# Kernel optimization log

Measured on AMD Instinct MI355X. Metric: run time of the kernel, lower is better.

## Reference

```python
import jax, jax.numpy as jnp
import numpy as np

B, S, D, H = 2, 2048, 1024, 16
DK = D // H


def setup_inputs() -> dict:
    key = jax.random.key(0)
    ks = jax.random.split(key, 9)
    w_scale = 0.02  # small init for linear weights
    return {
        "query": jax.random.normal(ks[0], (B, S, D), jnp.float32),
        "key": jax.random.normal(ks[1], (B, S, D), jnp.float32),
        "value": jax.random.normal(ks[2], (B, S, D), jnp.float32),
        "mask": jax.random.randint(ks[3], (B, 1, S, S), 0, 2).astype(bool),
        "Wq": jax.random.normal(ks[4], (D, D), jnp.float32) * w_scale,
        "bq": jnp.zeros((D,), jnp.float32),
        "Wk": jax.random.normal(ks[5], (D, D), jnp.float32) * w_scale,
        "bk": jnp.zeros((D,), jnp.float32),
        "Wv": jax.random.normal(ks[6], (D, D), jnp.float32) * w_scale,
        "bv": jnp.zeros((D,), jnp.float32),
        "Wo": jax.random.normal(ks[7], (D, D), jnp.float32) * w_scale,
        "bo": jnp.zeros((D,), jnp.float32),
    }


def _split_heads(x):
    # [B,S,D] -> [B,H,S,DK]
    return x.reshape(B, S, H, DK).transpose(0, 2, 1, 3)


def reference(query, key, value, mask, Wq, bq, Wk, bk, Wv, bv, Wo, bo):
    Q = _split_heads(query @ Wq + bq)
    K = _split_heads(key @ Wk + bk)
    V = _split_heads(value @ Wv + bv)
    scores = jnp.einsum("bhqd,bhkd->bhqk", Q, K) / jnp.sqrt(jnp.float32(DK))
    scores = jnp.where(mask, -jnp.inf, scores)  # masked_fill(mask, -inf)
    attn_w = jax.nn.softmax(scores, axis=-1)
    attn_w = jnp.nan_to_num(attn_w, nan=0.0)  # rows fully masked -> 0
    out = jnp.einsum("bhqk,bhkd->bhqd", attn_w, V)
    out = out.transpose(0, 2, 1, 3).reshape(B, S, D)
    return out @ Wo + bo
```

## Files before the change

kernel.cpp:

```cpp
#include <hip/hip_runtime.h>
#include <hip/hip_bf16.h>
#include <cmath>
#include <cstdint>
#include <cstddef>

#define B_  2
#define S_  2048
#define D_  1024
#define H_  16
#define DK_ 64
#define NEG_BIG (-1e30f)
#define QSCALE 0.1803368801111204f

typedef __attribute__((ext_vector_type(8))) short bf16x8;
typedef __attribute__((ext_vector_type(4))) float f32x4;
typedef __attribute__((ext_vector_type(16))) float f32x16;

static __device__ __forceinline__ unsigned short f2bf(float f) {
  __hip_bfloat16 h = __float2bfloat16(f);
  return *reinterpret_cast<unsigned short*>(&h);
}

static __device__ __forceinline__ unsigned cvtpk(float lo, float hi) {
  unsigned d;
  asm("v_cvt_pk_bf16_f32 %0, %1, %2" : "=v"(d) : "v"(lo), "v"(hi));
  return d;
}
static __device__ __forceinline__ float vexp2(float x) {
  float r;
  asm("v_exp_f32 %0, %1" : "=v"(r) : "v"(x));
  return r;
}
#define SWAP32(a, b) asm("v_permlane32_swap_b32 %0, %1" : "+v"(a), "+v"(b))

typedef __attribute__((address_space(3))) unsigned int lds_u32;
typedef __attribute__((address_space(1))) const unsigned int glb_u32;

__global__ void pack_mask_kernel(const int* __restrict__ mask,
                                 unsigned* __restrict__ bits) {
  const int t = blockIdx.x * 256 + threadIdx.x;
  const unsigned long long ball = __ballot(mask[t] != 0);
  const int lane = threadIdx.x & 63;
  if ((lane & 31) == 0)
    bits[t >> 5] = (lane == 0) ? (unsigned)ball : (unsigned)(ball >> 32);
}

__global__ __launch_bounds__(256) void transpose_w_kernel(
    const float* __restrict__ w0, const float* __restrict__ w1,
    const float* __restrict__ w2, const float* __restrict__ w3,
    unsigned short* __restrict__ t0, unsigned short* __restrict__ t1,
    unsigned short* __restrict__ t2, unsigned short* __restrict__ t3) {
  __shared__ unsigned short tile[32][33];
  const int z = blockIdx.z;
  const float* W = (z == 0) ? w0 : (z == 1) ? w1 : (z == 2) ? w2 : w3;
  unsigned short* Wt = (z == 0) ? t0 : (z == 1) ? t1 : (z == 2) ? t2 : t3;
  const int r0 = blockIdx.y * 32, c0 = blockIdx.x * 32;
  const int t = threadIdx.x;
  {
    const int r = t >> 3, c4 = (t & 7) * 4;
    float4 v = *reinterpret_cast<const float4*>(&W[(size_t)(r0 + r) * D_ + c0 + c4]);
    tile[c4 + 0][r] = f2bf(v.x);
    tile[c4 + 1][r] = f2bf(v.y);
    tile[c4 + 2][r] = f2bf(v.z);
    tile[c4 + 3][r] = f2bf(v.w);
  }
  __syncthreads();
  {
    const int n = t >> 3, k4 = (t & 7) * 4;
    ushort4 o = {tile[n][k4 + 0], tile[n][k4 + 1], tile[n][k4 + 2], tile[n][k4 + 3]};
    *reinterpret_cast<ushort4*>(&Wt[(size_t)(c0 + n) * D_ + r0 + k4]) = o;
  }
}

__global__ __launch_bounds__(256) void qkv_gemm_kernel(
    const float* __restrict__ qa, const float* __restrict__ ka,
    const float* __restrict__ va, const unsigned short* __restrict__ wtq,
    const unsigned short* __restrict__ wtk, const unsigned short* __restrict__ wtv,
    const float* __restrict__ bq, const float* __restrict__ bk,
    const float* __restrict__ bv, unsigned short* __restrict__ Qh,
    unsigned short* __restrict__ Kh, unsigned short* __restrict__ VT) {
  constexpr int K = D_;
  __shared__ __attribute__((aligned(16))) unsigned short as_[128 * 32];
  __shared__ __attribute__((aligned(16))) unsigned short bs_[128 * 32];
  const int z = blockIdx.z;
  const float* A = (z == 0) ? qa : (z == 1) ? ka : va;
  const unsigned short* Wt = (z == 0) ? wtq : (z == 1) ? wtk : wtv;
  const float* bias = (z == 0) ? bq : (z == 1) ? bk : bv;

  const int bm = blockIdx.x * 128, bn = blockIdx.y * 128;
  const int t = threadIdx.x, wv = t >> 6, lane = t & 63;
  const int r = lane & 15, g = lane >> 4;
  const int wr = (wv >> 1) * 64, wc = (wv & 1) * 64;
  const int srow = 16 * wv + (lane >> 2);
  const int scol = (lane & 3) * 8;
  const int ar0 = t >> 2, ak0 = (t & 3) * 8;
  const int ar1 = (t + 256) >> 2, ak1 = ak0;

  f32x4 acc[4][4] = {};

  for (int k0 = 0; k0 < K; k0 += 32) {
    const float4* ap0 = reinterpret_cast<const float4*>(&A[(size_t)(bm + ar0) * K + k0 + ak0]);
    const float4* ap1 = reinterpret_cast<const float4*>(&A[(size_t)(bm + ar1) * K + k0 + ak1]);
    float4 a0 = ap0[0], a1 = ap0[1];
    float4 a2 = ap1[0], a3 = ap1[1];
    __syncthreads();
    __builtin_amdgcn_global_load_lds(
        (glb_u32*)&Wt[(size_t)(bn + srow) * K + k0 + scol],
        (lds_u32*)(bs_ + wv * 512), 16, 0, 0);
    __builtin_amdgcn_global_load_lds(
        (glb_u32*)&Wt[(size_t)(bn + 64 + srow) * K + k0 + scol],
        (lds_u32*)(bs_ + wv * 512 + 2048), 16, 0, 0);
    union { unsigned u[4]; bf16x8 v; } w0, w1;
    w0.u[0] = cvtpk(a0.x, a0.y); w0.u[1] = cvtpk(a0.z, a0.w);
    w0.u[2] = cvtpk(a1.x, a1.y); w0.u[3] = cvtpk(a1.z, a1.w);
    w1.u[0] = cvtpk(a2.x, a2.y); w1.u[1] = cvtpk(a2.z, a2.w);
    w1.u[2] = cvtpk(a3.x, a3.y); w1.u[3] = cvtpk(a3.z, a3.w);
    *reinterpret_cast<bf16x8*>(&as_[(size_t)t * 8]) = w0.v;
    *reinterpret_cast<bf16x8*>(&as_[(size_t)(t + 256) * 8]) = w1.v;
    __syncthreads();

    bf16x8 a[4], bfr[4];
#pragma unroll
    for (int mf = 0; mf < 4; ++mf)
      a[mf] = *reinterpret_cast<const bf16x8*>(&as_[(wr + 16 * mf + r) * 32 + 8 * g]);
#pragma unroll
    for (int nf = 0; nf < 4; ++nf)
      bfr[nf] = *reinterpret_cast<const bf16x8*>(&bs_[(wc + 16 * nf + r) * 32 + 8 * g]);
#pragma unroll
    for (int mf = 0; mf < 4; ++mf)
#pragma unroll
      for (int nf = 0; nf < 4; ++nf)
        acc[mf][nf] = __builtin_amdgcn_mfma_f32_16x16x32_bf16(a[mf], bfr[nf],
                                                              acc[mf][nf], 0, 0, 0);
  }

#pragma unroll
  for (int mf = 0; mf < 4; ++mf)
#pragma unroll
    for (int nf = 0; nf < 4; ++nf)
#pragma unroll
      for (int reg = 0; reg < 4; ++reg) {
        const int row = bm + wr + 16 * mf + 4 * g + reg;
        const int col = bn + wc + 16 * nf + r;
        const float v = acc[mf][nf][reg] + bias[col];
        const int bb = row >> 11, s = row & (S_ - 1);
        const int h = col >> 6, dk = col & (DK_ - 1);
        if (z == 0)
          Qh[(((size_t)(bb * H_ + h)) * S_ + s) * DK_ + dk] = f2bf(v * QSCALE);
        else if (z == 1)
          Kh[(((size_t)(bb * H_ + h)) * S_ + s) * DK_ + dk] = f2bf(v);
        else
          VT[(((size_t)(bb * H_ + h)) * DK_ + dk) * S_ + s] = f2bf(v);
      }
}

__global__ __launch_bounds__(256) void out_gemm_kernel(
    const unsigned short* __restrict__ A, const unsigned short* __restrict__ Wt,
    const float* __restrict__ bias, float* __restrict__ Cout) {
  constexpr int K = D_;
  __shared__ __attribute__((aligned(16))) unsigned short as_[128 * 32];
  __shared__ __attribute__((aligned(16))) unsigned short bs_[128 * 32];
  const int bm = blockIdx.x * 128, bn = blockIdx.y * 128;
  const int t = threadIdx.x, wv = t >> 6, lane = t & 63;
  const int r = lane & 15, g = lane >> 4;
  const int wr = (wv >> 1) * 64, wc = (wv & 1) * 64;
  const int srow = 16 * wv + (lane >> 2);
  const int scol = (lane & 3) * 8;

  f32x4 acc[4][4] = {};

  for (int k0 = 0; k0 < K; k0 += 32) {
    __syncthreads();
    __builtin_amdgcn_global_load_lds(
        (glb_u32*)&A[(size_t)(bm + srow) * K + k0 + scol],
        (lds_u32*)(as_ + wv * 512), 16, 0, 0);
    __builtin_amdgcn_global_load_lds(
        (glb_u32*)&A[(size_t)(bm + 64 + srow) * K + k0 + scol],
        (lds_u32*)(as_ + wv * 512 + 2048), 16, 0, 0);
    __builtin_amdgcn_global_load_lds(
        (glb_u32*)&Wt[(size_t)(bn + srow) * K + k0 + scol],
        (lds_u32*)(bs_ + wv * 512), 16, 0, 0);
    __builtin_amdgcn_global_load_lds(
        (glb_u32*)&Wt[(size_t)(bn + 64 + srow) * K + k0 + scol],
        (lds_u32*)(bs_ + wv * 512 + 2048), 16, 0, 0);
    __syncthreads();

    bf16x8 a[4], bfr[4];
#pragma unroll
    for (int mf = 0; mf < 4; ++mf)
      a[mf] = *reinterpret_cast<const bf16x8*>(&as_[(wr + 16 * mf + r) * 32 + 8 * g]);
#pragma unroll
    for (int nf = 0; nf < 4; ++nf)
      bfr[nf] = *reinterpret_cast<const bf16x8*>(&bs_[(wc + 16 * nf + r) * 32 + 8 * g]);
#pragma unroll
    for (int mf = 0; mf < 4; ++mf)
#pragma unroll
      for (int nf = 0; nf < 4; ++nf)
        acc[mf][nf] = __builtin_amdgcn_mfma_f32_16x16x32_bf16(a[mf], bfr[nf],
                                                              acc[mf][nf], 0, 0, 0);
  }

#pragma unroll
  for (int mf = 0; mf < 4; ++mf)
#pragma unroll
    for (int nf = 0; nf < 4; ++nf)
#pragma unroll
      for (int reg = 0; reg < 4; ++reg) {
        const int row = bm + wr + 16 * mf + 4 * g + reg;
        const int col = bn + wc + 16 * nf + r;
        Cout[(size_t)row * D_ + col] = acc[mf][nf][reg] + bias[col];
      }
}

__global__ __launch_bounds__(256) void attn_mfma_kernel(
    const unsigned short* __restrict__ Qh, const unsigned short* __restrict__ Kh,
    const unsigned short* __restrict__ VT, const unsigned* __restrict__ mbits,
    unsigned short* __restrict__ ctx) {
  __shared__ float mlds[4][32];
  __shared__ float llds[4][32];
  __shared__ float olds[3][2][16][64];

  const int flat = blockIdx.x;
  const int bh = (flat & 7) * 4 + ((flat >> 3) & 3);
  const int qblk = flat >> 5;
  const int b = bh >> 4, h = bh & 15;
  const int kh = threadIdx.x >> 6, lane = threadIdx.x & 63;
  const int ql = lane & 31, hi = lane >> 5;
  const int qrow = qblk * 32 + ql;

  const unsigned short* Qrow = &Qh[((size_t)bh * S_ + qrow) * DK_];
  bf16x8 qf[4];
#pragma unroll
  for (int i = 0; i < 4; ++i)
    qf[i] = *(const bf16x8*)&Qrow[16 * i + 8 * hi];

  const unsigned short* Khead = &Kh[(size_t)bh * S_ * DK_];
  const unsigned short* Vhead = &VT[(size_t)bh * DK_ * S_];

  f32x16 o0 = {}, o1 = {};
  float m = NEG_BIG, l = 0.f;

  const unsigned short* kbase = Khead + ((size_t)(kh * 512 + ql)) * DK_ + 8 * hi;
  const unsigned short* vb0 = Vhead + (size_t)ql * S_ + kh * 512 + 8 * hi;
  const unsigned short* vb1 = vb0 + (size_t)32 * S_;
  const unsigned* mp = &mbits[((size_t)b * S_ + qrow) * (S_ / 32) + kh * 16];

  bf16x8 kc0[4], kc1[4];
#pragma unroll
  for (int i = 0; i < 4; ++i) {
    kc0[i] = *(const bf16x8*)(kbase + 16 * i);
    kc1[i] = *(const bf16x8*)(kbase + 2048 + 16 * i);
  }
  kbase += 4096;

#pragma unroll 1
  for (int it = 0; it < 8; ++it) {
    const uint2 mw = *reinterpret_cast<const uint2*>(mp);
    mp += 2;
    bf16x8 vf0[4], vf1[4];
#pragma unroll
    for (int kk = 0; kk < 4; ++kk) {
      vf0[kk] = *(const bf16x8*)(vb0 + kk * 16);
      vf1[kk] = *(const bf16x8*)(vb1 + kk * 16);
    }
    vb0 += 64;
    vb1 += 64;

    f32x16 sc0 = {}, sc1 = {};
#pragma unroll
    for (int i = 0; i < 4; ++i)
      sc0 = __builtin_amdgcn_mfma_f32_32x32x16_bf16(kc0[i], qf[i], sc0, 0, 0, 0);
#pragma unroll
    for (int i = 0; i < 4; ++i)
      sc1 = __builtin_amdgcn_mfma_f32_32x32x16_bf16(kc1[i], qf[i], sc1, 0, 0, 0);

    if (it < 7) {
#pragma unroll
      for (int i = 0; i < 4; ++i) {
        kc0[i] = *(const bf16x8*)(kbase + 16 * i);
        kc1[i] = *(const bf16x8*)(kbase + 2048 + 16 * i);
      }
      kbase += 4096;
    }

    const unsigned m0 = mw.x >> (4 * hi), m1 = mw.y >> (4 * hi);
#pragma unroll
    for (int reg = 0; reg < 16; ++reg) {
      const int creg = (reg & 3) + 8 * (reg >> 2);
      if ((m0 >> creg) & 1u) sc0[reg] = NEG_BIG;
      if ((m1 >> creg) & 1u) sc1[reg] = NEG_BIG;
    }

    float px;
    {
      float t0 = fmaxf(fmaxf(sc0[0], sc0[1]), sc0[2]);
      float t1 = fmaxf(fmaxf(sc0[3], sc0[4]), sc0[5]);
      float t2 = fmaxf(fmaxf(sc0[6], sc0[7]), sc0[8]);
      float t3 = fmaxf(fmaxf(sc0[9], sc0[10]), sc0[11]);
      float t4 = fmaxf(fmaxf(sc0[12], sc0[13]), sc0[14]);
      float t5 = fmaxf(fmaxf(sc0[15], sc1[0]), sc1[1]);
      float t6 = fmaxf(fmaxf(sc1[2], sc1[3]), sc1[4]);
      float t7 = fmaxf(fmaxf(sc1[5], sc1[6]), sc1[7]);
      float t8 = fmaxf(fmaxf(sc1[8], sc1[9]), sc1[10]);
      float t9 = fmaxf(fmaxf(sc1[11], sc1[12]), sc1[13]);
      float ta = fmaxf(sc1[14], sc1[15]);
      float u0 = fmaxf(fmaxf(t0, t1), t2);
      float u1 = fmaxf(fmaxf(t3, t4), t5);
      float u2 = fmaxf(fmaxf(t6, t7), t8);
      float u3 = fmaxf(t9, ta);
      px = fmaxf(fmaxf(u0, u1), fmaxf(u2, u3));
    }
    px = fmaxf(px, __shfl_xor(px, 32));

    if (!__all(px - m <= 11.f)) {
      const float mn = fmaxf(m, px);
      const float al = vexp2(m - mn);
      m = mn;
      l *= al;
#pragma unroll
      for (int reg = 0; reg < 16; ++reg) { o0[reg] *= al; o1[reg] *= al; }
    }

#pragma unroll
    for (int reg = 0; reg < 16; ++reg) {
      sc0[reg] = vexp2(sc0[reg] - m);
      sc1[reg] = vexp2(sc1[reg] - m);
    }
    {
      float s0 = (sc0[0] + sc0[1]) + (sc0[2] + sc0[3]);
      float s1 = (sc0[4] + sc0[5]) + (sc0[6] + sc0[7]);
      float s2 = (sc0[8] + sc0[9]) + (sc0[10] + sc0[11]);
      float s3 = (sc0[12] + sc0[13]) + (sc0[14] + sc0[15]);
      float s4 = (sc1[0] + sc1[1]) + (sc1[2] + sc1[3]);
      float s5 = (sc1[4] + sc1[5]) + (sc1[6] + sc1[7]);
      float s6 = (sc1[8] + sc1[9]) + (sc1[10] + sc1[11]);
      float s7 = (sc1[12] + sc1[13]) + (sc1[14] + sc1[15]);
      float rs = ((s0 + s1) + (s2 + s3)) + ((s4 + s5) + (s6 + s7));
      rs += __shfl_xor(rs, 32);
      l += rs;
    }

    unsigned w0 = cvtpk(sc0[0], sc0[1]), w2p = cvtpk(sc0[4], sc0[5]);
    unsigned w1 = cvtpk(sc0[2], sc0[3]), w3p = cvtpk(sc0[6], sc0[7]);
    unsigned x0 = cvtpk(sc0[8], sc0[9]), x2p = cvtpk(sc0[12], sc0[13]);
    unsigned x1 = cvtpk(sc0[10], sc0[11]), x3p = cvtpk(sc0[14], sc0[15]);
    unsigned y0 = cvtpk(sc1[0], sc1[1]), y2p = cvtpk(sc1[4], sc1[5]);
    unsigned y1 = cvtpk(sc1[2], sc1[3]), y3p = cvtpk(sc1[6], sc1[7]);
    unsigned z0 = cvtpk(sc1[8], sc1[9]), z2p = cvtpk(sc1[12], sc1[13]);
    unsigned z1 = cvtpk(sc1[10], sc1[11]), z3p = cvtpk(sc1[14], sc1[15]);
    SWAP32(w0, w2p); SWAP32(w1, w3p); SWAP32(x0, x2p); SWAP32(x1, x3p);
    SWAP32(y0, y2p); SWAP32(y1, y3p); SWAP32(z0, z2p); SWAP32(z1, z3p);
    union { unsigned u[4]; bf16x8 v; } pu0, pu1, pu2, pu3;
    pu0.u[0] = w0; pu0.u[1] = w1; pu0.u[2] = w2p; pu0.u[3] = w3p;
    pu1.u[0] = x0; pu1.u[1] = x1; pu1.u[2] = x2p; pu1.u[3] = x3p;
    pu2.u[0] = y0; pu2.u[1] = y1; pu2.u[2] = y2p; pu2.u[3] = y3p;
    pu3.u[0] = z0; pu3.u[1] = z1; pu3.u[2] = z2p; pu3.u[3] = z3p;

    o0 = __builtin_amdgcn_mfma_f32_32x32x16_bf16(pu0.v, vf0[0], o0, 0, 0, 0);
    o0 = __builtin_amdgcn_mfma_f32_32x32x16_bf16(pu1.v, vf0[1], o0, 0, 0, 0);
    o0 = __builtin_amdgcn_mfma_f32_32x32x16_bf16(pu2.v, vf0[2], o0, 0, 0, 0);
    o0 = __builtin_amdgcn_mfma_f32_32x32x16_bf16(pu3.v, vf0[3], o0, 0, 0, 0);
    o1 = __builtin_amdgcn_mfma_f32_32x32x16_bf16(pu0.v, vf1[0], o1, 0, 0, 0);
    o1 = __builtin_amdgcn_mfma_f32_32x32x16_bf16(pu1.v, vf1[1], o1, 0, 0, 0);
    o1 = __builtin_amdgcn_mfma_f32_32x32x16_bf16(pu2.v, vf1[2], o1, 0, 0, 0);
    o1 = __builtin_amdgcn_mfma_f32_32x32x16_bf16(pu3.v, vf1[3], o1, 0, 0, 0);
  }

  if (lane < 32) {
    mlds[kh][ql] = m;
    llds[kh][ql] = l;
  }
  if (kh < 3) {
#pragma unroll
    for (int reg = 0; reg < 16; ++reg) {
      olds[kh][0][reg][lane] = o0[reg];
      olds[kh][1][reg][lane] = o1[reg];
    }
  }
  __syncthreads();
  if (kh == 3) {
#pragma unroll
    for (int reg = 0; reg < 16; ++reg) {
      const int crow = (reg & 3) + 8 * (reg >> 2) + 4 * hi;
      const float m0 = mlds[0][crow], m1 = mlds[1][crow];
      const float m2 = mlds[2][crow], m3 = mlds[3][crow];
      const float ms = fmaxf(fmaxf(m0, m1), fmaxf(m2, m3));
      const float f0 = vexp2(m0 - ms), f1 = vexp2(m1 - ms);
      const float f2 = vexp2(m2 - ms), f3 = vexp2(m3 - ms);
      const float ls = llds[0][crow] * f0 + llds[1][crow] * f1 +
                       llds[2][crow] * f2 + llds[3][crow] * f3;
      const float inv = (ms == NEG_BIG) ? 0.f : 1.f / ls;
      const float v0 = (olds[0][0][reg][lane] * f0 + olds[1][0][reg][lane] * f1 +
                        olds[2][0][reg][lane] * f2 + o0[reg] * f3) * inv;
      const float v1 = (olds[0][1][reg][lane] * f0 + olds[1][1][reg][lane] * f1 +
                        olds[2][1][reg][lane] * f2 + o1[reg] * f3) * inv;
      const int q = qblk * 32 + crow;
      unsigned short* cp = &ctx[((size_t)(b * S_ + q)) * D_ + h * DK_];
      cp[ql] = f2bf(v0);
      cp[32 + ql] = f2bf(v1);
    }
  }
}

extern "C" void kernel_launch(void* const* d_in, const int* in_sizes, int n_in,
                              void* d_out, int out_size, void* d_ws,
                              size_t ws_size, hipStream_t stream) {
  const float* query = (const float*)d_in[0];
  const float* key   = (const float*)d_in[1];
  const float* value = (const float*)d_in[2];
  const int*   mask  = (const int*)d_in[3];
  const float* Wq = (const float*)d_in[4];
  const float* bq = (const float*)d_in[5];
  const float* Wk = (const float*)d_in[6];
  const float* bk = (const float*)d_in[7];
  const float* Wv = (const float*)d_in[8];
  const float* bv = (const float*)d_in[9];
  const float* Wo = (const float*)d_in[10];
  const float* bo = (const float*)d_in[11];
  float* out = (float*)d_out;

  const size_t nElem = (size_t)B_ * S_ * D_;
  const size_t wElem = (size_t)D_ * D_;
  unsigned short* ws = (unsigned short*)d_ws;
  unsigned short* wtq  = ws;
  unsigned short* wtk  = wtq + wElem;
  unsigned short* wtv  = wtk + wElem;
  unsigned short* wto  = wtv + wElem;
  unsigned short* Qh   = wto + wElem;
  unsigned short* Kh   = Qh + nElem;
  unsigned short* VT   = Kh + nElem;
  unsigned short* ctxb = VT + nElem;
  unsigned* mbits = (unsigned*)(ctxb + nElem);

  pack_mask_kernel<<<(B_ * S_ * S_) / 256, 256, 0, stream>>>(mask, mbits);
  {
    dim3 grid(32, 32, 4);
    transpose_w_kernel<<<grid, 256, 0, stream>>>(Wq, Wk, Wv, Wo, wtq, wtk, wtv, wto);
  }
  {
    dim3 grid(32, 8, 3);
    qkv_gemm_kernel<<<grid, 256, 0, stream>>>(query, key, value, wtq, wtk, wtv,
                                              bq, bk, bv, Qh, Kh, VT);
  }
  attn_mfma_kernel<<<2048, 256, 0, stream>>>(Qh, Kh, VT, mbits, ctxb);
  {
    dim3 grid(32, 8);
    out_gemm_kernel<<<grid, 256, 0, stream>>>(ctxb, wto, bo, out);
  }
}
```

Measured before the change: 354.2 us.

## Restructure pipeline: pre-convert inputs, transposed V GEMM, 64-row attention tiles, smaller out tiles

```diff
diff --git a/kernel.cpp b/kernel.cpp
--- a/kernel.cpp
+++ b/kernel.cpp
@@ -43,6 +43,25 @@
   const int lane = threadIdx.x & 63;
   if ((lane & 31) == 0)
     bits[t >> 5] = (lane == 0) ? (unsigned)ball : (unsigned)(ball >> 32);
+}
+
+__global__ void cvt_f32_bf16_kernel(const float* __restrict__ q,
+                                    const float* __restrict__ k,
+                                    const float* __restrict__ v,
+                                    unsigned short* __restrict__ qo,
+                                    unsigned short* __restrict__ ko,
+                                    unsigned short* __restrict__ vo, int n8) {
+  int i = blockIdx.x * blockDim.x + threadIdx.x;
+  if (i >= n8) return;
+  const float* in = (blockIdx.y == 0) ? q : (blockIdx.y == 1) ? k : v;
+  unsigned short* out = (blockIdx.y == 0) ? qo : (blockIdx.y == 1) ? ko : vo;
+  const float4* p = reinterpret_cast<const float4*>(in) + (size_t)i * 2;
+  float4 a = p[0], b = p[1];
+  ushort4 o0 = {f2bf(a.x), f2bf(a.y), f2bf(a.z), f2bf(a.w)};
+  ushort4 o1 = {f2bf(b.x), f2bf(b.y), f2bf(b.z), f2bf(b.w)};
+  ushort4* o = reinterpret_cast<ushort4*>(out) + (size_t)i * 2;
+  o[0] = o0;
+  o[1] = o1;
 }
 
 __global__ __launch_bounds__(256) void transpose_w_kernel(
@@ -73,19 +92,17 @@
 }
 
 __global__ __launch_bounds__(256) void qkv_gemm_kernel(
-    const float* __restrict__ qa, const float* __restrict__ ka,
-    const float* __restrict__ va, const unsigned short* __restrict__ wtq,
-    const unsigned short* __restrict__ wtk, const unsigned short* __restrict__ wtv,
+    const unsigned short* __restrict__ qb, const unsigned short* __restrict__ kb,
+    const unsigned short* __restrict__ wtq, const unsigned short* __restrict__ wtk,
     const float* __restrict__ bq, const float* __restrict__ bk,
-    const float* __restrict__ bv, unsigned short* __restrict__ Qh,
-    unsigned short* __restrict__ Kh, unsigned short* __restrict__ VT) {
+    unsigned short* __restrict__ Qh, unsigned short* __restrict__ Kh) {
   constexpr int K = D_;
   __shared__ __attribute__((aligned(16))) unsigned short as_[128 * 32];
   __shared__ __attribute__((aligned(16))) unsigned short bs_[128 * 32];
   const int z = blockIdx.z;
-  const float* A = (z == 0) ? qa : (z == 1) ? ka : va;
-  const unsigned short* Wt = (z == 0) ? wtq : (z == 1) ? wtk : wtv;
-  const float* bias = (z == 0) ? bq : (z == 1) ? bk : bv;
+  const unsigned short* A = (z == 0) ? qb : kb;
+  const unsigned short* Wt = (z == 0) ? wtq : wtk;
+  const float* bias = (z == 0) ? bq : bk;
 
   const int bm = blockIdx.x * 128, bn = blockIdx.y * 128;
   const int t = threadIdx.x, wv = t >> 6, lane = t & 63;
@@ -93,30 +110,23 @@
   const int wr = (wv >> 1) * 64, wc = (wv & 1) * 64;
   const int srow = 16 * wv + (lane >> 2);
   const int scol = (lane & 3) * 8;
-  const int ar0 = t >> 2, ak0 = (t & 3) * 8;
-  const int ar1 = (t + 256) >> 2, ak1 = ak0;
 
   f32x4 acc[4][4] = {};
 
   for (int k0 = 0; k0 < K; k0 += 32) {
-    const float4* ap0 = reinterpret_cast<const float4*>(&A[(size_t)(bm + ar0) * K + k0 + ak0]);
-    const float4* ap1 = reinterpret_cast<const float4*>(&A[(size_t)(bm + ar1) * K + k0 + ak1]);
-    float4 a0 = ap0[0], a1 = ap0[1];
-    float4 a2 = ap1[0], a3 = ap1[1];
     __syncthreads();
+    __builtin_amdgcn_global_load_lds(
+        (glb_u32*)&A[(size_t)(bm + srow) * K + k0 + scol],
+        (lds_u32*)(as_ + wv * 512), 16, 0, 0);
+    __builtin_amdgcn_global_load_lds(
+        (glb_u32*)&A[(size_t)(bm + 64 + srow) * K + k0 + scol],
+        (lds_u32*)(as_ + wv * 512 + 2048), 16, 0, 0);
     __builtin_amdgcn_global_load_lds(
         (glb_u32*)&Wt[(size_t)(bn + srow) * K + k0 + scol],
         (lds_u32*)(bs_ + wv * 512), 16, 0, 0);
     __builtin_amdgcn_global_load_lds(
         (glb_u32*)&Wt[(size_t)(bn + 64 + srow) * K + k0 + scol],
         (lds_u32*)(bs_ + wv * 512 + 2048), 16, 0, 0);
-    union { unsigned u[4]; bf16x8 v; } w0, w1;
-    w0.u[0] = cvtpk(a0.x, a0.y); w0.u[1] = cvtpk(a0.z, a0.w);
-    w0.u[2] = cvtpk(a1.x, a1.y); w0.u[3] = cvtpk(a1.z, a1.w);
-    w1.u[0] = cvtpk(a2.x, a2.y); w1.u[1] = cvtpk(a2.z, a2.w);
-    w1.u[2] = cvtpk(a3.x, a3.y); w1.u[3] = cvtpk(a3.z, a3.w);
-    *reinterpret_cast<bf16x8*>(&as_[(size_t)t * 8]) = w0.v;
-    *reinterpret_cast<bf16x8*>(&as_[(size_t)(t + 256) * 8]) = w1.v;
     __syncthreads();
 
     bf16x8 a[4], bfr[4];
@@ -147,20 +157,19 @@
         const int h = col >> 6, dk = col & (DK_ - 1);
         if (z == 0)
           Qh[(((size_t)(bb * H_ + h)) * S_ + s) * DK_ + dk] = f2bf(v * QSCALE);
-        else if (z == 1)
+        else
           Kh[(((size_t)(bb * H_ + h)) * S_ + s) * DK_ + dk] = f2bf(v);
-        else
-          VT[(((size_t)(bb * H_ + h)) * DK_ + dk) * S_ + s] = f2bf(v);
       }
 }
 
-__global__ __launch_bounds__(256) void out_gemm_kernel(
-    const unsigned short* __restrict__ A, const unsigned short* __restrict__ Wt,
-    const float* __restrict__ bias, float* __restrict__ Cout) {
+__global__ __launch_bounds__(256) void vt_gemm_kernel(
+    const unsigned short* __restrict__ Wt, const unsigned short* __restrict__ act,
+    const float* __restrict__ bias, unsigned short* __restrict__ VT) {
   constexpr int K = D_;
   __shared__ __attribute__((aligned(16))) unsigned short as_[128 * 32];
   __shared__ __attribute__((aligned(16))) unsigned short bs_[128 * 32];
-  const int bm = blockIdx.x * 128, bn = blockIdx.y * 128;
+  const int bm = blockIdx.x * 128;
+  const int bn = blockIdx.y * 128;
   const int t = threadIdx.x, wv = t >> 6, lane = t & 63;
   const int r = lane & 15, g = lane >> 4;
   const int wr = (wv >> 1) * 64, wc = (wv & 1) * 64;
@@ -172,11 +181,69 @@
   for (int k0 = 0; k0 < K; k0 += 32) {
     __syncthreads();
     __builtin_amdgcn_global_load_lds(
+        (glb_u32*)&Wt[(size_t)(bm + srow) * K + k0 + scol],
+        (lds_u32*)(as_ + wv * 512), 16, 0, 0);
+    __builtin_amdgcn_global_load_lds(
+        (glb_u32*)&Wt[(size_t)(bm + 64 + srow) * K + k0 + scol],
+        (lds_u32*)(as_ + wv * 512 + 2048), 16, 0, 0);
+    __builtin_amdgcn_global_load_lds(
+        (glb_u32*)&act[(size_t)(bn + srow) * K + k0 + scol],
+        (lds_u32*)(bs_ + wv * 512), 16, 0, 0);
+    __builtin_amdgcn_global_load_lds(
+        (glb_u32*)&act[(size_t)(bn + 64 + srow) * K + k0 + scol],
+        (lds_u32*)(bs_ + wv * 512 + 2048), 16, 0, 0);
+    __syncthreads();
+
+    bf16x8 a[4], bfr[4];
+#pragma unroll
+    for (int mf = 0; mf < 4; ++mf)
+      a[mf] = *reinterpret_cast<const bf16x8*>(&as_[(wr + 16 * mf + r) * 32 + 8 * g]);
+#pragma unroll
+    for (int nf = 0; nf < 4; ++nf)
+      bfr[nf] = *reinterpret_cast<const bf16x8*>(&bs_[(wc + 16 * nf + r) * 32 + 8 * g]);
+#pragma unroll
+    for (int mf = 0; mf < 4; ++mf)
+#pragma unroll
+      for (int nf = 0; nf < 4; ++nf)
+        acc[mf][nf] = __builtin_amdgcn_mfma_f32_16x16x32_bf16(a[mf], bfr[nf],
+                                                              acc[mf][nf], 0, 0, 0);
+  }
+
+#pragma unroll
+  for (int mf = 0; mf < 4; ++mf)
+#pragma unroll
+    for (int nf = 0; nf < 4; ++nf)
+#pragma unroll
+      for (int reg = 0; reg < 4; ++reg) {
+        const int row = bm + wr + 16 * mf + 4 * g + reg;
+        const int col = bn + wc + 16 * nf + r;
+        const float v = acc[mf][nf][reg] + bias[row];
+        const int h = row >> 6, dk = row & (DK_ - 1);
+        const int bb = col >> 11, s = col & (S_ - 1);
+        VT[(((size_t)(bb * H_ + h)) * DK_ + dk) * S_ + s] = f2bf(v);
+      }
+}
+
+__global__ __launch_bounds__(256) void out_gemm_kernel(
+    const unsigned short* __restrict__ A, const unsigned short* __restrict__ Wt,
+    const float* __restrict__ bias, float* __restrict__ Cout) {
+  constexpr int K = D_;
+  __shared__ __attribute__((aligned(16))) unsigned short as_[64 * 32];
+  __shared__ __attribute__((aligned(16))) unsigned short bs_[128 * 32];
+  const int bm = blockIdx.x * 64, bn = blockIdx.y * 128;
+  const int t = threadIdx.x, wv = t >> 6, lane = t & 63;
+  const int r = lane & 15, g = lane >> 4;
+  const int wr = (wv >> 1) * 32, wc = (wv & 1) * 64;
+  const int srow = 16 * wv + (lane >> 2);
+  const int scol = (lane & 3) * 8;
+
+  f32x4 acc[2][4] = {};
+
+  for (int k0 = 0; k0 < K; k0 += 32) {
+    __syncthreads();
+    __builtin_amdgcn_global_load_lds(
         (glb_u32*)&A[(size_t)(bm + srow) * K + k0 + scol],
         (lds_u32*)(as_ + wv * 512), 16, 0, 0);
-    __builtin_amdgcn_global_load_lds(
-        (glb_u32*)&A[(size_t)(bm + 64 + srow) * K + k0 + scol],
-        (lds_u32*)(as_ + wv * 512 + 2048), 16, 0, 0);
     __builtin_amdgcn_global_load_lds(
         (glb_u32*)&Wt[(size_t)(bn + srow) * K + k0 + scol],
         (lds_u32*)(bs_ + wv * 512), 16, 0, 0);
@@ -185,15 +252,15 @@
         (lds_u32*)(bs_ + wv * 512 + 2048), 16, 0, 0);
     __syncthreads();
 
-    bf16x8 a[4], bfr[4];
-#pragma unroll
-    for (int mf = 0; mf < 4; ++mf)
+    bf16x8 a[2], bfr[4];
+#pragma unroll
+    for (int mf = 0; mf < 2; ++mf)
       a[mf] = *reinterpret_cast<const bf16x8*>(&as_[(wr + 16 * mf + r) * 32 + 8 * g]);
 #pragma unroll
     for (int nf = 0; nf < 4; ++nf)
       bfr[nf] = *reinterpret_cast<const bf16x8*>(&bs_[(wc + 16 * nf + r) * 32 + 8 * g]);
 #pragma unroll
-    for (int mf = 0; mf < 4; ++mf)
+    for (int mf = 0; mf < 2; ++mf)
 #pragma unroll
       for (int nf = 0; nf < 4; ++nf)
         acc[mf][nf] = __builtin_amdgcn_mfma_f32_16x16x32_bf16(a[mf], bfr[nf],
@@ -201,7 +268,7 @@
   }
 
 #pragma unroll
-  for (int mf = 0; mf < 4; ++mf)
+  for (int mf = 0; mf < 2; ++mf)
 #pragma unroll
     for (int nf = 0; nf < 4; ++nf)
 #pragma unroll
@@ -212,13 +279,13 @@
       }
 }
 
-__global__ __launch_bounds__(256) void attn_mfma_kernel(
+__global__ __launch_bounds__(256, 2) void attn_mfma_kernel(
     const unsigned short* __restrict__ Qh, const unsigned short* __restrict__ Kh,
     const unsigned short* __restrict__ VT, const unsigned* __restrict__ mbits,
     unsigned short* __restrict__ ctx) {
-  __shared__ float mlds[4][32];
-  __shared__ float llds[4][32];
-  __shared__ float olds[3][2][16][64];
+  __shared__ float mlds[2][4][32];
+  __shared__ float llds[2][4][32];
+  __shared__ float olds[2][3][2][16][64];
 
   const int flat = blockIdx.x;
   const int bh = (flat & 7) * 4 + ((flat >> 3) & 3);
@@ -226,26 +293,33 @@
   const int b = bh >> 4, h = bh & 15;
   const int kh = threadIdx.x >> 6, lane = threadIdx.x & 63;
   const int ql = lane & 31, hi = lane >> 5;
-  const int qrow = qblk * 32 + ql;
-
-  const unsigned short* Qrow = &Qh[((size_t)bh * S_ + qrow) * DK_];
-  bf16x8 qf[4];
-#pragma unroll
-  for (int i = 0; i < 4; ++i)
-    qf[i] = *(const bf16x8*)&Qrow[16 * i + 8 * hi];
+  const int qrowA = qblk * 64 + ql;
+  const int qrowB = qrowA + 32;
+
+  bf16x8 qfA[4], qfB[4];
+  {
+    const unsigned short* QrA = &Qh[((size_t)bh * S_ + qrowA) * DK_];
+    const unsigned short* QrB = &Qh[((size_t)bh * S_ + qrowB) * DK_];
+#pragma unroll
+    for (int i = 0; i < 4; ++i) {
+      qfA[i] = *(const bf16x8*)&QrA[16 * i + 8 * hi];
+      qfB[i] = *(const bf16x8*)&QrB[16 * i + 8 * hi];
+    }
+  }
 
   const unsigned short* Khead = &Kh[(size_t)bh * S_ * DK_];
   const unsigned short* Vhead = &VT[(size_t)bh * DK_ * S_];
 
-  f32x16 o0 = {}, o1 = {};
-  float m = NEG_BIG, l = 0.f;
+  f32x16 oA0 = {}, oA1 = {}, oB0 = {}, oB1 = {};
+  float mA = NEG_BIG, lA = 0.f, mB = NEG_BIG, lB = 0.f;
 
   const unsigned short* kbase = Khead + ((size_t)(kh * 512 + ql)) * DK_ + 8 * hi;
   const unsigned short* vb0 = Vhead + (size_t)ql * S_ + kh * 512 + 8 * hi;
   const unsigned short* vb1 = vb0 + (size_t)32 * S_;
-  const unsigned* mp = &mbits[((size_t)b * S_ + qrow) * (S_ / 32) + kh * 16];
-
-  bf16x8 kc0[4], kc1[4];
+  const unsigned* mpA = &mbits[((size_t)b * S_ + qrowA) * (S_ / 32) + kh * 16];
+  const unsigned* mpB = &mbits[((size_t)b * S_ + qrowB) * (S_ / 32) + kh * 16];
+
+  bf16x8 kc0[4], kc1[4], vf0[4], vf1[4];
 #pragma unroll
   for (int i = 0; i < 4; ++i) {
     kc0[i] = *(const bf16x8*)(kbase + 16 * i);
@@ -253,57 +327,28 @@
   }
   kbase += 4096;
 
-#pragma unroll 1
-  for (int it = 0; it < 8; ++it) {
-    const uint2 mw = *reinterpret_cast<const uint2*>(mp);
-    mp += 2;
-    bf16x8 vf0[4], vf1[4];
-#pragma unroll
-    for (int kk = 0; kk < 4; ++kk) {
-      vf0[kk] = *(const bf16x8*)(vb0 + kk * 16);
-      vf1[kk] = *(const bf16x8*)(vb1 + kk * 16);
-    }
-    vb0 += 64;
-    vb1 += 64;
-
-    f32x16 sc0 = {}, sc1 = {};
-#pragma unroll
-    for (int i = 0; i < 4; ++i)
-      sc0 = __builtin_amdgcn_mfma_f32_32x32x16_bf16(kc0[i], qf[i], sc0, 0, 0, 0);
-#pragma unroll
-    for (int i = 0; i < 4; ++i)
-      sc1 = __builtin_amdgcn_mfma_f32_32x32x16_bf16(kc1[i], qf[i], sc1, 0, 0, 0);
-
-    if (it < 7) {
-#pragma unroll
-      for (int i = 0; i < 4; ++i) {
-        kc0[i] = *(const bf16x8*)(kbase + 16 * i);
-        kc1[i] = *(const bf16x8*)(kbase + 2048 + 16 * i);
-      }
-      kbase += 4096;
-    }
-
-    const unsigned m0 = mw.x >> (4 * hi), m1 = mw.y >> (4 * hi);
+  auto process = [&](f32x16& s0, f32x16& s1, const uint2 mw, float& m, float& l,
+                     f32x16& q0, f32x16& q1) {
+    const unsigned w0m = mw.x >> (4 * hi), w1m = mw.y >> (4 * hi);
 #pragma unroll
     for (int reg = 0; reg < 16; ++reg) {
       const int creg = (reg & 3) + 8 * (reg >> 2);
-      if ((m0 >> creg) & 1u) sc0[reg] = NEG_BIG;
-      if ((m1 >> creg) & 1u) sc1[reg] = NEG_BIG;
-    }
-
+      if ((w0m >> creg) & 1u) s0[reg] = NEG_BIG;
+      if ((w1m >> creg) & 1u) s1[reg] = NEG_BIG;
+    }
     float px;
     {
-      float t0 = fmaxf(fmaxf(sc0[0], sc0[1]), sc0[2]);
-      float t1 = fmaxf(fmaxf(sc0[3], sc0[4]), sc0[5]);
-      float t2 = fmaxf(fmaxf(sc0[6], sc0[7]), sc0[8]);
-      float t3 = fmaxf(fmaxf(sc0[9], sc0[10]), sc0[11]);
-      float t4 = fmaxf(fmaxf(sc0[12], sc0[13]), sc0[14]);
-      float t5 = fmaxf(fmaxf(sc0[15], sc1[0]), sc1[1]);
-      float t6 = fmaxf(fmaxf(sc1[2], sc1[3]), sc1[4]);
-      float t7 = fmaxf(fmaxf(sc1[5], sc1[6]), sc1[7]);
-      float t8 = fmaxf(fmaxf(sc1[8], sc1[9]), sc1[10]);
-      float t9 = fmaxf(fmaxf(sc1[11], sc1[12]), sc1[13]);
-      float ta = fmaxf(sc1[14], sc1[15]);
+      float t0 = fmaxf(fmaxf(s0[0], s0[1]), s0[2]);
+      float t1 = fmaxf(fmaxf(s0[3], s0[4]), s0[5]);
+      float t2 = fmaxf(fmaxf(s0[6], s0[7]), s0[8]);
+      float t3 = fmaxf(fmaxf(s0[9], s0[10]), s0[11]);
+      float t4 = fmaxf(fmaxf(s0[12], s0[13]), s0[14]);
+      float t5 = fmaxf(fmaxf(s0[15], s1[0]), s1[1]);
+      float t6 = fmaxf(fmaxf(s1[2], s1[3]), s1[4]);
+      float t7 = fmaxf(fmaxf(s1[5], s1[6]), s1[7]);
+      float t8 = fmaxf(fmaxf(s1[8], s1[9]), s1[10]);
+      float t9 = fmaxf(fmaxf(s1[11], s1[12]), s1[13]);
+      float ta = fmaxf(s1[14], s1[15]);
       float u0 = fmaxf(fmaxf(t0, t1), t2);
       float u1 = fmaxf(fmaxf(t3, t4), t5);
       float u2 = fmaxf(fmaxf(t6, t7), t8);
@@ -311,43 +356,40 @@
       px = fmaxf(fmaxf(u0, u1), fmaxf(u2, u3));
     }
     px = fmaxf(px, __shfl_xor(px, 32));
-
     if (!__all(px - m <= 11.f)) {
       const float mn = fmaxf(m, px);
       const float al = vexp2(m - mn);
       m = mn;
       l *= al;
 #pragma unroll
-      for (int reg = 0; reg < 16; ++reg) { o0[reg] *= al; o1[reg] *= al; }
-    }
-
+      for (int reg = 0; reg < 16; ++reg) { q0[reg] *= al; q1[reg] *= al; }
+    }
 #pragma unroll
     for (int reg = 0; reg < 16; ++reg) {
-      sc0[reg] = vexp2(sc0[reg] - m);
-      sc1[reg] = vexp2(sc1[reg] - m);
+      s0[reg] = vexp2(s0[reg] - m);
+      s1[reg] = vexp2(s1[reg] - m);
     }
     {
-      float s0 = (sc0[0] + sc0[1]) + (sc0[2] + sc0[3]);
-      float s1 = (sc0[4] + sc0[5]) + (sc0[6] + sc0[7]);
-      float s2 = (sc0[8] + sc0[9]) + (sc0[10] + sc0[11]);
-      float s3 = (sc0[12] + sc0[13]) + (sc0[14] + sc0[15]);
-      float s4 = (sc1[0] + sc1[1]) + (sc1[2] + sc1[3]);
-      float s5 = (sc1[4] + sc1[5]) + (sc1[6] + sc1[7]);
-      float s6 = (sc1[8] + sc1[9]) + (sc1[10] + sc1[11]);
-      float s7 = (sc1[12] + sc1[13]) + (sc1[14] + sc1[15]);
-      float rs = ((s0 + s1) + (s2 + s3)) + ((s4 + s5) + (s6 + s7));
+      float a0 = (s0[0] + s0[1]) + (s0[2] + s0[3]);
+      float a1 = (s0[4] + s0[5]) + (s0[6] + s0[7]);
+      float a2 = (s0[8] + s0[9]) + (s0[10] + s0[11]);
+      float a3 = (s0[12] + s0[13]) + (s0[14] + s0[15]);
+      float a4 = (s1[0] + s1[1]) + (s1[2] + s1[3]);
+      float a5 = (s1[4] + s1[5]) + (s1[6] + s1[7]);
+      float a6 = (s1[8] + s1[9]) + (s1[10] + s1[11]);
+      float a7 = (s1[12] + s1[13]) + (s1[14] + s1[15]);
+      float rs = ((a0 + a1) + (a2 + a3)) + ((a4 + a5) + (a6 + a7));
       rs += __shfl_xor(rs, 32);
       l += rs;
     }
-
-    unsigned w0 = cvtpk(sc0[0], sc0[1]), w2p = cvtpk(sc0[4], sc0[5]);
-    unsigned w1 = cvtpk(sc0[2], sc0[3]), w3p = cvtpk(sc0[6], sc0[7]);
-    unsigned x0 = cvtpk(sc0[8], sc0[9]), x2p = cvtpk(sc0[12], sc0[13]);
-    unsigned x1 = cvtpk(sc0[10], sc0[11]), x3p = cvtpk(sc0[14], sc0[15]);
-    unsigned y0 = cvtpk(sc1[0], sc1[1]), y2p = cvtpk(sc1[4], sc1[5]);
-    unsigned y1 = cvtpk(sc1[2], sc1[3]), y3p = cvtpk(sc1[6], sc1[7]);
-    unsigned z0 = cvtpk(sc1[8], sc1[9]), z2p = cvtpk(sc1[12], sc1[13]);
-    unsigned z1 = cvtpk(sc1[10], sc1[11]), z3p = cvtpk(sc1[14], sc1[15]);
+    unsigned w0 = cvtpk(s0[0], s0[1]), w2p = cvtpk(s0[4], s0[5]);
+    unsigned w1 = cvtpk(s0[2], s0[3]), w3p = cvtpk(s0[6], s0[7]);
+    unsigned x0 = cvtpk(s0[8], s0[9]), x2p = cvtpk(s0[12], s0[13]);
+    unsigned x1 = cvtpk(s0[10], s0[11]), x3p = cvtpk(s0[14], s0[15]);
+    unsigned y0 = cvtpk(s1[0], s1[1]), y2p = cvtpk(s1[4], s1[5]);
+    unsigned y1 = cvtpk(s1[2], s1[3]), y3p = cvtpk(s1[6], s1[7]);
+    unsigned z0 = cvtpk(s1[8], s1[9]), z2p = cvtpk(s1[12], s1[13]);
+    unsigned z1 = cvtpk(s1[10], s1[11]), z3p = cvtpk(s1[14], s1[15]);
     SWAP32(w0, w2p); SWAP32(w1, w3p); SWAP32(x0, x2p); SWAP32(x1, x3p);
     SWAP32(y0, y2p); SWAP32(y1, y3p); SWAP32(z0, z2p); SWAP32(z1, z3p);
     union { unsigned u[4]; bf16x8 v; } pu0, pu1, pu2, pu3;
@@ -355,49 +397,107 @@
     pu1.u[0] = x0; pu1.u[1] = x1; pu1.u[2] = x2p; pu1.u[3] = x3p;
     pu2.u[0] = y0; pu2.u[1] = y1; pu2.u[2] = y2p; pu2.u[3] = y3p;
     pu3.u[0] = z0; pu3.u[1] = z1; pu3.u[2] = z2p; pu3.u[3] = z3p;
-
-    o0 = __builtin_amdgcn_mfma_f32_32x32x16_bf16(pu0.v, vf0[0], o0, 0, 0, 0);
-    o0 = __builtin_amdgcn_mfma_f32_32x32x16_bf16(pu1.v, vf0[1], o0, 0, 0, 0);
-    o0 = __builtin_amdgcn_mfma_f32_32x32x16_bf16(pu2.v, vf0[2], o0, 0, 0, 0);
-    o0 = __builtin_amdgcn_mfma_f32_32x32x16_bf16(pu3.v, vf0[3], o0, 0, 0, 0);
-    o1 = __builtin_amdgcn_mfma_f32_32x32x16_bf16(pu0.v, vf1[0], o1, 0, 0, 0);
-    o1 = __builtin_amdgcn_mfma_f32_32x32x16_bf16(pu1.v, vf1[1], o1, 0, 0, 0);
-    o1 = __builtin_amdgcn_mfma_f32_32x32x16_bf16(pu2.v, vf1[2], o1, 0, 0, 0);
-    o1 = __builtin_amdgcn_mfma_f32_32x32x16_bf16(pu3.v, vf1[3], o1, 0, 0, 0);
+    __builtin_amdgcn_s_setprio(1);
+    q0 = __builtin_amdgcn_mfma_f32_32x32x16_bf16(pu0.v, vf0[0], q0, 0, 0, 0);
+    q0 = __builtin_amdgcn_mfma_f32_32x32x16_bf16(pu1.v, vf0[1], q0, 0, 0, 0);
+    q0 = __builtin_amdgcn_mfma_f32_32x32x16_bf16(pu2.v, vf0[2], q0, 0, 0, 0);
+    q0 = __builtin_amdgcn_mfma_f32_32x32x16_bf16(pu3.v, vf0[3], q0, 0, 0, 0);
+    q1 = __builtin_amdgcn_mfma_f32_32x32x16_bf16(pu0.v, vf1[0], q1, 0, 0, 0);
+    q1 = __builtin_amdgcn_mfma_f32_32x32x16_bf16(pu1.v, vf1[1], q1, 0, 0, 0);
+    q1 = __builtin_amdgcn_mfma_f32_32x32x16_bf16(pu2.v, vf1[2], q1, 0, 0, 0);
+    q1 = __builtin_amdgcn_mfma_f32_32x32x16_bf16(pu3.v, vf1[3], q1, 0, 0, 0);
+    __builtin_amdgcn_s_setprio(0);
+  };
+
+#pragma unroll 1
+  for (int it = 0; it < 8; ++it) {
+    const uint2 mwA = *reinterpret_cast<const uint2*>(mpA);
+    const uint2 mwB = *reinterpret_cast<const uint2*>(mpB);
+    mpA += 2;
+    mpB += 2;
+#pragma unroll
+    for (int kk = 0; kk < 4; ++kk) {
+      vf0[kk] = *(const bf16x8*)(vb0 + kk * 16);
+      vf1[kk] = *(const bf16x8*)(vb1 + kk * 16);
+    }
+    vb0 += 64;
+    vb1 += 64;
+
+    f32x16 sA0 = {}, sA1 = {};
+    __builtin_amdgcn_s_setprio(1);
+#pragma unroll
+    for (int i = 0; i < 4; ++i)
+      sA0 = __builtin_amdgcn_mfma_f32_32x32x16_bf16(kc0[i], qfA[i], sA0, 0, 0, 0);
+#pragma unroll
+    for (int i = 0; i < 4; ++i)
+      sA1 = __builtin_amdgcn_mfma_f32_32x32x16_bf16(kc1[i], qfA[i], sA1, 0, 0, 0);
+    __builtin_amdgcn_s_setprio(0);
+    process(sA0, sA1, mwA, mA, lA, oA0, oA1);
+
+    f32x16 sB0 = {}, sB1 = {};
+    __builtin_amdgcn_s_setprio(1);
+#pragma unroll
+    for (int i = 0; i < 4; ++i)
+      sB0 = __builtin_amdgcn_mfma_f32_32x32x16_bf16(kc0[i], qfB[i], sB0, 0, 0, 0);
+#pragma unroll
+    for (int i = 0; i < 4; ++i)
+      sB1 = __builtin_amdgcn_mfma_f32_32x32x16_bf16(kc1[i], qfB[i], sB1, 0, 0, 0);
+    __builtin_amdgcn_s_setprio(0);
+
+    if (it < 7) {
+#pragma unroll
+      for (int i = 0; i < 4; ++i) {
+        kc0[i] = *(const bf16x8*)(kbase + 16 * i);
+        kc1[i] = *(const bf16x8*)(kbase + 2048 + 16 * i);
+      }
+      kbase += 4096;
+    }
+    process(sB0, sB1, mwB, mB, lB, oB0, oB1);
   }
 
   if (lane < 32) {
-    mlds[kh][ql] = m;
-    llds[kh][ql] = l;
+    mlds[0][kh][ql] = mA;
+    llds[0][kh][ql] = lA;
+    mlds[1][kh][ql] = mB;
+    llds[1][kh][ql] = lB;
   }
   if (kh < 3) {
 #pragma unroll
     for (int reg = 0; reg < 16; ++reg) {
-      olds[kh][0][reg][lane] = o0[reg];
-      olds[kh][1][reg][lane] = o1[reg];
+      olds[0][kh][0][reg][lane] = oA0[reg];
+      olds[0][kh][1][reg][lane] = oA1[reg];
+      olds[1][kh][0][reg][lane] = oB0[reg];
+      olds[1][kh][1][reg][lane] = oB1[reg];
     }
   }
   __syncthreads();
   if (kh == 3) {
 #pragma unroll
-    for (int reg = 0; reg < 16; ++reg) {
-      const int crow = (reg & 3) + 8 * (reg >> 2) + 4 * hi;
-      const float m0 = mlds[0][crow], m1 = mlds[1][crow];
-      const float m2 = mlds[2][crow], m3 = mlds[3][crow];
-      const float ms = fmaxf(fmaxf(m0, m1), fmaxf(m2, m3));
-      const float f0 = vexp2(m0 - ms), f1 = vexp2(m1 - ms);
-      const float f2 = vexp2(m2 - ms), f3 = vexp2(m3 - ms);
-      const float ls = llds[0][crow] * f0 + llds[1][crow] * f1 +
-                       llds[2][crow] * f2 + llds[3][crow] * f3;
-      const float inv = (ms == NEG_BIG) ? 0.f : 1.f / ls;
-      const float v0 = (olds[0][0][reg][lane] * f0 + olds[1][0][reg][lane] * f1 +
-                        olds[2][0][reg][lane] * f2 + o0[reg] * f3) * inv;
-      const float v1 = (olds[0][1][reg][lane] * f0 + olds[1][1][reg][lane] * f1 +
-                        olds[2][1][reg][lane] * f2 + o1[reg] * f3) * inv;
-      const int q = qblk * 32 + crow;
-      unsigned short* cp = &ctx[((size_t)(b * S_ + q)) * D_ + h * DK_];
-      cp[ql] = f2bf(v0);
-      cp[32 + ql] = f2bf(v1);
+    for (int tile = 0; tile < 2; ++tile) {
+      const f32x16& r0 = tile ? oB0 : oA0;
+      const f32x16& r1 = tile ? oB1 : oA1;
+#pragma unroll
+      for (int reg = 0; reg < 16; ++reg) {
+        const int crow = (reg & 3) + 8 * (reg >> 2) + 4 * hi;
+        const float m0 = mlds[tile][0][crow], m1 = mlds[tile][1][crow];
+        const float m2 = mlds[tile][2][crow], m3 = mlds[tile][3][crow];
+        const float ms = fmaxf(fmaxf(m0, m1), fmaxf(m2, m3));
+        const float f0 = vexp2(m0 - ms), f1 = vexp2(m1 - ms);
+        const float f2 = vexp2(m2 - ms), f3 = vexp2(m3 - ms);
+        const float ls = llds[tile][0][crow] * f0 + llds[tile][1][crow] * f1 +
+                         llds[tile][2][crow] * f2 + llds[tile][3][crow] * f3;
+        const float inv = (ms == NEG_BIG) ? 0.f : 1.f / ls;
+        const float v0 = (olds[tile][0][0][reg][lane] * f0 +
+                          olds[tile][1][0][reg][lane] * f1 +
+                          olds[tile][2][0][reg][lane] * f2 + r0[reg] * f3) * inv;
+        const float v1 = (olds[tile][0][1][reg][lane] * f0 +
+                          olds[tile][1][1][reg][lane] * f1 +
+                          olds[tile][2][1][reg][lane] * f2 + r1[reg] * f3) * inv;
+        const int q = qblk * 64 + tile * 32 + crow;
+        unsigned short* cp = &ctx[((size_t)(b * S_ + q)) * D_ + h * DK_];
+        cp[ql] = f2bf(v0);
+        cp[32 + ql] = f2bf(v1);
+      }
     }
   }
 }
@@ -422,7 +522,10 @@
   const size_t nElem = (size_t)B_ * S_ * D_;
   const size_t wElem = (size_t)D_ * D_;
   unsigned short* ws = (unsigned short*)d_ws;
-  unsigned short* wtq  = ws;
+  unsigned short* qb   = ws;
+  unsigned short* kb   = qb + nElem;
+  unsigned short* vb   = kb + nElem;
+  unsigned short* wtq  = vb + nElem;
   unsigned short* wtk  = wtq + wElem;
   unsigned short* wtv  = wtk + wElem;
   unsigned short* wto  = wtv + wElem;
@@ -434,17 +537,25 @@
 
   pack_mask_kernel<<<(B_ * S_ * S_) / 256, 256, 0, stream>>>(mask, mbits);
   {
+    const int n8 = (int)(nElem / 8);
+    dim3 grid((n8 + 255) / 256, 3);
+    cvt_f32_bf16_kernel<<<grid, 256, 0, stream>>>(query, key, value, qb, kb, vb, n8);
+  }
+  {
     dim3 grid(32, 32, 4);
     transpose_w_kernel<<<grid, 256, 0, stream>>>(Wq, Wk, Wv, Wo, wtq, wtk, wtv, wto);
   }
   {
-    dim3 grid(32, 8, 3);
-    qkv_gemm_kernel<<<grid, 256, 0, stream>>>(query, key, value, wtq, wtk, wtv,
-                                              bq, bk, bv, Qh, Kh, VT);
-  }
-  attn_mfma_kernel<<<2048, 256, 0, stream>>>(Qh, Kh, VT, mbits, ctxb);
-  {
-    dim3 grid(32, 8);
+    dim3 grid(32, 8, 2);
+    qkv_gemm_kernel<<<grid, 256, 0, stream>>>(qb, kb, wtq, wtk, bq, bk, Qh, Kh);
+  }
+  {
+    dim3 grid(8, 32);
+    vt_gemm_kernel<<<grid, 256, 0, stream>>>(wtv, vb, bv, VT);
+  }
+  attn_mfma_kernel<<<1024, 256, 0, stream>>>(Qh, Kh, VT, mbits, ctxb);
+  {
+    dim3 grid(64, 8);
     out_gemm_kernel<<<grid, 256, 0, stream>>>(ctxb, wto, bo, out);
   }
 }
```

Result: faster. 309.6 us (-12.6%).
